# Performance work log

Hardware: AMD Instinct MI355X
Metric: run time of the kernel (lower is better)

## Reference

```python
import jax, jax.numpy as jnp
import numpy as np

NUM_GROUPS = 32
EPS = 1e-6


def group_norm(x, w, b):
    # x: (B, C, L); normalize per group of C//32 channels over (channels-in-group, L)
    B, C, L = x.shape
    xg = x.reshape(B, NUM_GROUPS, C // NUM_GROUPS, L)
    mean = jnp.mean(xg, axis=(2, 3), keepdims=True)
    var = jnp.var(xg, axis=(2, 3), keepdims=True)
    xn = ((xg - mean) * jax.lax.rsqrt(var + EPS)).reshape(B, C, L)
    return xn * w[None, :, None] + b[None, :, None]


def conv1x1(x, w, b):
    # 1x1 Conv1d == channel-mixing linear. x: (B,C,L), w: (O,C), b: (O,)
    return jnp.einsum('oc,bcl->bol', w, x) + b[None, :, None]


def setup_inputs() -> dict:
    key = jax.random.key(0)
    ks = jax.random.split(key, 6)
    B, C, L = 8, 512, 2048
    s = 1.0 / np.sqrt(C)
    return {
        'x': jax.random.normal(ks[0], (B, C, L), dtype=jnp.float32),
        'gn_w': jnp.ones((C,), jnp.float32),
        'gn_b': jnp.zeros((C,), jnp.float32),
        'wq': jax.random.normal(ks[1], (C, C), dtype=jnp.float32) * s,
        'bq': jnp.zeros((C,), jnp.float32),
        'wk': jax.random.normal(ks[2], (C, C), dtype=jnp.float32) * s,
        'bk': jnp.zeros((C,), jnp.float32),
        'wv': jax.random.normal(ks[3], (C, C), dtype=jnp.float32) * s,
        'bv': jnp.zeros((C,), jnp.float32),
        'wo': jax.random.normal(ks[4], (C, C), dtype=jnp.float32) * s,
        'bo': jnp.zeros((C,), jnp.float32),
    }


def reference(x, gn_w, gn_b, wq, bq, wk, bk, wv, bv, wo, bo):
    B, C, L = x.shape
    h = group_norm(x, gn_w, gn_b)
    q = conv1x1(h, wq, bq)  # (B,C,L)
    k = conv1x1(h, wk, bk)
    v = conv1x1(h, wv, bv)
    scale = jnp.asarray(C, x.dtype) ** -0.5
    # scores over length: w[b,i,j] = sum_c q[b,c,i] k[b,c,j]
    w_ = jnp.einsum('bci,bcj->bij', q, k) * scale
    w_ = jax.nn.softmax(w_, axis=-1)
    # h[b,c,i] = sum_j w[b,i,j] v[b,c,j]
    h = jnp.einsum('bij,bcj->bci', w_, v)
    h = conv1x1(h, wo, bo)
    return x + h
```

## Files before the change

### kernel.cpp

```cpp
#include <hip/hip_runtime.h>
#include <math.h>

#define BATCH 8
#define CH 512
#define LEN 2048
#define NG 32
#define CPG 16

typedef unsigned short u16;
typedef __bf16 bf16x8 __attribute__((ext_vector_type(8)));
typedef float f32x16 __attribute__((ext_vector_type(16)));

__device__ __forceinline__ u16 f2bf(float f) {
    union { float f; unsigned u; } c; c.f = f;
    unsigned r = c.u + 0x7fffu + ((c.u >> 16) & 1u);
    return (u16)(r >> 16);
}
__device__ __forceinline__ float bf2f(u16 h) {
    union { unsigned u; float f; } c; c.u = ((unsigned)h) << 16;
    return c.f;
}
__device__ __forceinline__ void gload16(const u16* g, u16* l) {
    __builtin_amdgcn_global_load_lds(
        (const __attribute__((address_space(1))) unsigned int*)g,
        (__attribute__((address_space(3))) unsigned int*)l, 16, 0, 0);
}

__global__ __launch_bounds__(256) void zerof4(float4* __restrict__ p) {
    p[blockIdx.x * 256 + threadIdx.x] = make_float4(0.f, 0.f, 0.f, 0.f);
}

__global__ __launch_bounds__(256) void wconv4(const float* __restrict__ w0, const float* __restrict__ w1,
                                              const float* __restrict__ w2, const float* __restrict__ w3,
                                              u16* __restrict__ o0, u16* __restrict__ o1,
                                              u16* __restrict__ o2, u16* __restrict__ o3) {
    const float* s; u16* d;
    switch (blockIdx.y) {
        case 0: s = w0; d = o0; break;
        case 1: s = w1; d = o1; break;
        case 2: s = w2; d = o2; break;
        default: s = w3; d = o3; break;
    }
    const int i = blockIdx.x * 256 + threadIdx.x;
    float4 f = ((const float4*)s)[i];
    ushort4 o = make_ushort4(f2bf(f.x), f2bf(f.y), f2bf(f.z), f2bf(f.w));
    ((ushort4*)d)[i] = o;
}

__global__ __launch_bounds__(256) void gn_stats(const float* __restrict__ x,
                                                const float* __restrict__ gw,
                                                const float* __restrict__ gb,
                                                float* __restrict__ gnA,
                                                float* __restrict__ gnB) {
    const int b = blockIdx.x >> 5, g = blockIdx.x & 31;
    const float4* xp = (const float4*)(x + ((size_t)b * CH + (size_t)g * CPG) * LEN);
    float s = 0.f, s2 = 0.f;
    for (int i = threadIdx.x; i < (CPG * LEN) / 4; i += 256) {
        float4 v = xp[i];
        s += v.x + v.y + v.z + v.w;
        s2 = fmaf(v.x, v.x, fmaf(v.y, v.y, fmaf(v.z, v.z, fmaf(v.w, v.w, s2))));
    }
    #pragma unroll
    for (int off = 32; off > 0; off >>= 1) {
        s  += __shfl_down(s, off, 64);
        s2 += __shfl_down(s2, off, 64);
    }
    __shared__ float sm[2][4];
    const int lane = threadIdx.x & 63, wv = threadIdx.x >> 6;
    if (lane == 0) { sm[0][wv] = s; sm[1][wv] = s2; }
    __syncthreads();
    if (threadIdx.x < CPG) {
        const float S  = sm[0][0] + sm[0][1] + sm[0][2] + sm[0][3];
        const float S2 = sm[1][0] + sm[1][1] + sm[1][2] + sm[1][3];
        const float mean = S * (1.f / (CPG * LEN));
        const float var  = S2 * (1.f / (CPG * LEN)) - mean * mean;
        const float rstd = rsqrtf(var + 1e-6f);
        const int c = g * CPG + threadIdx.x;
        const float sc = rstd * gw[c];
        gnA[b * CH + c] = sc;
        gnB[b * CH + c] = gb[c] - mean * sc;
    }
}

__global__ __launch_bounds__(256) void gn_apply_t(const float* __restrict__ x,
                                                  const float* __restrict__ gnA,
                                                  const float* __restrict__ gnB,
                                                  u16* __restrict__ Ht) {
    __shared__ float tile[64][65];
    const int b = blockIdx.z, c0 = blockIdx.y * 64, l0 = blockIdx.x * 64;
    const int t = threadIdx.x, tl = t & 63, tr = t >> 6;
    #pragma unroll 4
    for (int i = 0; i < 16; ++i) {
        const int c = tr + i * 4;
        const float a = gnA[b * CH + c0 + c];
        const float sh = gnB[b * CH + c0 + c];
        tile[c][tl] = x[((size_t)b * CH + c0 + c) * LEN + l0 + tl] * a + sh;
    }
    __syncthreads();
    #pragma unroll 4
    for (int i = 0; i < 16; ++i) {
        const int l = tr + i * 4;
        Ht[((size_t)b * LEN + l0 + l) * CH + c0 + tl] = f2bf(tile[tl][l]);
    }
}

#define EPI_QK   0
#define EPI_TBN  1
#define EPI_EXP  2
#define EPI_TNRM 3
#define EPI_FIN  4

template <int MODE>
__global__ __launch_bounds__(256) void gemm_bt(
    const u16* __restrict__ A, int lda, long long sA,
    const u16* __restrict__ B, int ldb, long long sB,
    void* __restrict__ Out, void* __restrict__ Out2,
    int ldo, long long sO,
    const float* __restrict__ bias, const float* __restrict__ bias2,
    const float* __restrict__ res, long long sR,
    float* __restrict__ rsum, long long sRS,
    int K, float alpha) {
    __shared__ u16 As[128 * 64];
    __shared__ u16 Bs[128 * 64];
    const int b = blockIdx.z;
    const int n0 = blockIdx.x * 128, m0 = blockIdx.y * 128;
    A += (size_t)b * sA;
    B += (size_t)b * sB;
    const int t = threadIdx.x;
    const int lane = t & 63, wid = t >> 6;

    const int rowL = t >> 3, kq = (t & 7) ^ (rowL & 7);
    const u16* gA[4];
    const u16* gB[4];
    u16* lA[4];
    u16* lB[4];
    #pragma unroll
    for (int g = 0; g < 4; ++g) {
        gA[g] = A + (size_t)(m0 + rowL + g * 32) * lda + kq * 8;
        gB[g] = B + (size_t)(n0 + rowL + g * 32) * ldb + kq * 8;
        lA[g] = As + t * 8 + g * 2048;
        lB[g] = Bs + t * 8 + g * 2048;
    }

    f32x16 acc[2][2];
    #pragma unroll
    for (int i = 0; i < 2; ++i)
        #pragma unroll
        for (int j = 0; j < 2; ++j)
            acc[i][j] = (f32x16)(0.f);

    const int col = lane & 31, half = lane >> 5;
    const int wm = (wid & 1) * 64, wn = (wid >> 1) * 64;
    const int mf = wm + col, nf = wn + col;
    const int mswz = mf & 7, nswz = nf & 7;

    for (int k0 = 0; k0 < K; k0 += 64) {
        #pragma unroll
        for (int g = 0; g < 4; ++g) {
            gload16(gA[g], lA[g]);
            gload16(gB[g], lB[g]);
            gA[g] += 64; gB[g] += 64;
        }
        __syncthreads();
        #pragma unroll
        for (int ks = 0; ks < 4; ++ks) {
            const int kcA = ((ks * 2 + half) ^ mswz) * 8;
            const int kcB = ((ks * 2 + half) ^ nswz) * 8;
            bf16x8 a0 = *(const bf16x8*)(As + (mf)      * 64 + kcA);
            bf16x8 a1 = *(const bf16x8*)(As + (mf + 32) * 64 + kcA);
            bf16x8 b0 = *(const bf16x8*)(Bs + (nf)      * 64 + kcB);
            bf16x8 b1 = *(const bf16x8*)(Bs + (nf + 32) * 64 + kcB);
            acc[0][0] = __builtin_amdgcn_mfma_f32_32x32x16_bf16(a0, b0, acc[0][0], 0, 0, 0);
            acc[0][1] = __builtin_amdgcn_mfma_f32_32x32x16_bf16(a0, b1, acc[0][1], 0, 0, 0);
            acc[1][0] = __builtin_amdgcn_mfma_f32_32x32x16_bf16(a1, b0, acc[1][0], 0, 0, 0);
            acc[1][1] = __builtin_amdgcn_mfma_f32_32x32x16_bf16(a1, b1, acc[1][1], 0, 0, 0);
        }
        __syncthreads();
    }

    if (MODE == EPI_FIN) {
        float* O = (float*)Out + (size_t)b * sO;
        const float* R = res + (size_t)b * sR;
        #pragma unroll
        for (int im = 0; im < 2; ++im)
            #pragma unroll
            for (int g4 = 0; g4 < 4; ++g4) {
                const int mb = m0 + wm + im * 32 + g4 * 8 + half * 4;
                #pragma unroll
                for (int jn = 0; jn < 2; ++jn) {
                    const int n = n0 + wn + jn * 32 + col;
                    const float bb = bias[n];
                    const size_t base = (size_t)n * ldo + mb;
                    const float4 r4 = *(const float4*)&R[base];
                    float4 o4;
                    o4.x = acc[im][jn][g4 * 4 + 0] + bb + r4.x;
                    o4.y = acc[im][jn][g4 * 4 + 1] + bb + r4.y;
                    o4.z = acc[im][jn][g4 * 4 + 2] + bb + r4.z;
                    o4.w = acc[im][jn][g4 * 4 + 3] + bb + r4.w;
                    *(float4*)&O[base] = o4;
                }
            }
    } else if (MODE == EPI_EXP) {
        u16* O = (u16*)Out + (size_t)b * sO;
        float* RS = rsum + (size_t)b * sRS;
        float psum[2] = {0.f, 0.f};
        #pragma unroll
        for (int im = 0; im < 2; ++im)
            #pragma unroll
            for (int g4 = 0; g4 < 4; ++g4) {
                const int mb = m0 + wm + im * 32 + g4 * 8 + half * 4;
                #pragma unroll
                for (int jn = 0; jn < 2; ++jn) {
                    const int n = n0 + wn + jn * 32 + col;
                    u16 h0 = f2bf(__expf(acc[im][jn][g4 * 4 + 0] * alpha));
                    u16 h1 = f2bf(__expf(acc[im][jn][g4 * 4 + 1] * alpha));
                    u16 h2 = f2bf(__expf(acc[im][jn][g4 * 4 + 2] * alpha));
                    u16 h3 = f2bf(__expf(acc[im][jn][g4 * 4 + 3] * alpha));
                    psum[jn] += bf2f(h0) + bf2f(h1) + bf2f(h2) + bf2f(h3);
                    *(ushort4*)&O[(size_t)n * ldo + mb] = make_ushort4(h0, h1, h2, h3);
                }
            }
        #pragma unroll
        for (int jn = 0; jn < 2; ++jn) psum[jn] += __shfl_xor(psum[jn], 32, 64);
        if (half == 0) {
            #pragma unroll
            for (int jn = 0; jn < 2; ++jn)
                atomicAdd(&RS[n0 + wn + jn * 32 + col], psum[jn]);
        }
    } else {
        u16* O;
        const float* bi = bias;
        const float* RS = (MODE == EPI_TNRM) ? rsum + (size_t)b * sRS : nullptr;
        int mbase = m0 + wm;
        if (MODE == EPI_QK) {
            const bool hi = (m0 & 512) != 0;
            O  = (u16*)(hi ? Out2 : Out) + (size_t)b * sO;
            bi = hi ? bias2 : bias;
            mbase = (m0 & 511) + wm;
        } else {
            O = (u16*)Out + (size_t)b * sO;
        }
        float inv[2];
        if (MODE == EPI_TNRM) {
            inv[0] = 1.f / RS[n0 + wn + col];
            inv[1] = 1.f / RS[n0 + wn + 32 + col];
        }
        #pragma unroll
        for (int im = 0; im < 2; ++im)
            #pragma unroll
            for (int g4 = 0; g4 < 4; ++g4) {
                const int mb = mbase + im * 32 + g4 * 8 + half * 4;
                float4 bm = make_float4(0.f, 0.f, 0.f, 0.f);
                if (MODE == EPI_QK) bm = *(const float4*)&bi[mb];
                #pragma unroll
                for (int jn = 0; jn < 2; ++jn) {
                    const int n = n0 + wn + jn * 32 + col;
                    float v0 = acc[im][jn][g4 * 4 + 0];
                    float v1 = acc[im][jn][g4 * 4 + 1];
                    float v2 = acc[im][jn][g4 * 4 + 2];
                    float v3 = acc[im][jn][g4 * 4 + 3];
                    if (MODE == EPI_QK)  { v0 += bm.x; v1 += bm.y; v2 += bm.z; v3 += bm.w; }
                    if (MODE == EPI_TBN) { const float bb = bi[n]; v0 += bb; v1 += bb; v2 += bb; v3 += bb; }
                    if (MODE == EPI_TNRM) { v0 *= inv[jn]; v1 *= inv[jn]; v2 *= inv[jn]; v3 *= inv[jn]; }
                    ushort4 pk = make_ushort4(f2bf(v0), f2bf(v1), f2bf(v2), f2bf(v3));
                    *(ushort4*)&O[(size_t)n * ldo + mb] = pk;
                }
            }
    }
}

extern "C" void kernel_launch(void* const* d_in, const int* in_sizes, int n_in,
                              void* d_out, int out_size, void* d_ws, size_t ws_size,
                              hipStream_t stream) {
    const float* x    = (const float*)d_in[0];
    const float* gn_w = (const float*)d_in[1];
    const float* gn_b = (const float*)d_in[2];
    const float* wq   = (const float*)d_in[3];
    const float* bq   = (const float*)d_in[4];
    const float* wk   = (const float*)d_in[5];
    const float* bk   = (const float*)d_in[6];
    const float* wv   = (const float*)d_in[7];
    const float* bv   = (const float*)d_in[8];
    const float* wo   = (const float*)d_in[9];
    const float* bo   = (const float*)d_in[10];
    float* out = (float*)d_out;

    char* p = (char*)d_ws;
    const size_t WSZ = (size_t)CH * CH * 2;
    const size_t HSZ = (size_t)BATCH * CH * LEN * 2;
    u16* Wqk = (u16*)p; p += 2 * WSZ;
    u16* Wvb = (u16*)p; p += WSZ;
    u16* Wob = (u16*)p; p += WSZ;
    u16* Ht  = (u16*)p; p += HSZ;
    u16* Qt  = (u16*)p; p += HSZ;
    u16* Kt  = (u16*)p; p += HSZ;
    u16* Vb  = (u16*)p; p += HSZ;
    u16* Sb  = (u16*)p; p += (size_t)BATCH * LEN * LEN * 2;
    float* gnA = (float*)p; p += (size_t)BATCH * CH * 4;
    float* gnB = (float*)p; p += (size_t)BATCH * CH * 4;
    float* rowsum = (float*)p;

    const long long sH = (long long)LEN * CH;
    const long long sV = (long long)CH * LEN;
    const long long sS = (long long)LEN * LEN;
    const float scale = 0.04419417382415922f;

    wconv4<<<dim3(256, 4), 256, 0, stream>>>(wq, wk, wv, wo,
                                             Wqk, Wqk + (size_t)CH * CH, Wvb, Wob);
    gn_stats<<<BATCH * NG, 256, 0, stream>>>(x, gn_w, gn_b, gnA, gnB);
    gn_apply_t<<<dim3(LEN / 64, CH / 64, BATCH), 256, 0, stream>>>(x, gnA, gnB, Ht);
    zerof4<<<BATCH * LEN / 1024, 256, 0, stream>>>((float4*)rowsum);

    gemm_bt<EPI_QK><<<dim3(16, 8, 8), 256, 0, stream>>>(
        Wqk, CH, 0, Ht, CH, sH, Qt, Kt, CH, sH, bq, bk, nullptr, 0, nullptr, 0, CH, 0.f);
    gemm_bt<EPI_TBN><<<dim3(4, 16, 8), 256, 0, stream>>>(
        Ht, CH, sH, Wvb, CH, 0, Vb, nullptr, LEN, sV, bv, nullptr, nullptr, 0, nullptr, 0, CH, 0.f);
    gemm_bt<EPI_EXP><<<dim3(16, 16, 8), 256, 0, stream>>>(
        Kt, CH, sH, Qt, CH, sH, Sb, nullptr, LEN, sS, nullptr, nullptr, nullptr, 0, rowsum, LEN, CH, scale);
    gemm_bt<EPI_TNRM><<<dim3(16, 4, 8), 256, 0, stream>>>(
        Vb, LEN, sV, Sb, LEN, sS, Ht, nullptr, CH, sH, nullptr, nullptr, nullptr, 0, rowsum, LEN, LEN, 0.f);
    gemm_bt<EPI_FIN><<<dim3(4, 16, 8), 256, 0, stream>>>(
        Ht, CH, sH, Wob, CH, 0, out, nullptr, LEN, sV, bo, nullptr, x, sV, nullptr, 0, CH, 0.f);
}
```

Measured before the change: 301.8 us.

## Use 256x128 tile GEMM for QK projection and scores; merge prep kernels

Adds a gemm_big kernel with a 256x128 output tile (4x2 MFMA 32x32 fragments per wave) and uses it for the fused Q/K projection and the exp(QK^T) score GEMM. The larger tile raises arithmetic intensity and halves the block count for those launches. The weight conversion, group-norm statistics and rowsum zeroing are also merged into one prep launch to save launch overhead. The trade-offs are higher register and LDS use per block, which may lower occupancy, and fewer blocks per launch.

```diff
diff --git a/kernel.cpp b/kernel.cpp
--- a/kernel.cpp
+++ b/kernel.cpp
@@ -26,59 +26,57 @@
         (__attribute__((address_space(3))) unsigned int*)l, 16, 0, 0);
 }
 
-__global__ __launch_bounds__(256) void zerof4(float4* __restrict__ p) {
-    p[blockIdx.x * 256 + threadIdx.x] = make_float4(0.f, 0.f, 0.f, 0.f);
-}
-
-__global__ __launch_bounds__(256) void wconv4(const float* __restrict__ w0, const float* __restrict__ w1,
-                                              const float* __restrict__ w2, const float* __restrict__ w3,
-                                              u16* __restrict__ o0, u16* __restrict__ o1,
-                                              u16* __restrict__ o2, u16* __restrict__ o3) {
-    const float* s; u16* d;
-    switch (blockIdx.y) {
-        case 0: s = w0; d = o0; break;
-        case 1: s = w1; d = o1; break;
-        case 2: s = w2; d = o2; break;
-        default: s = w3; d = o3; break;
-    }
-    const int i = blockIdx.x * 256 + threadIdx.x;
-    float4 f = ((const float4*)s)[i];
-    ushort4 o = make_ushort4(f2bf(f.x), f2bf(f.y), f2bf(f.z), f2bf(f.w));
-    ((ushort4*)d)[i] = o;
-}
-
-__global__ __launch_bounds__(256) void gn_stats(const float* __restrict__ x,
-                                                const float* __restrict__ gw,
-                                                const float* __restrict__ gb,
-                                                float* __restrict__ gnA,
-                                                float* __restrict__ gnB) {
-    const int b = blockIdx.x >> 5, g = blockIdx.x & 31;
-    const float4* xp = (const float4*)(x + ((size_t)b * CH + (size_t)g * CPG) * LEN);
-    float s = 0.f, s2 = 0.f;
-    for (int i = threadIdx.x; i < (CPG * LEN) / 4; i += 256) {
-        float4 v = xp[i];
-        s += v.x + v.y + v.z + v.w;
-        s2 = fmaf(v.x, v.x, fmaf(v.y, v.y, fmaf(v.z, v.z, fmaf(v.w, v.w, s2))));
-    }
-    #pragma unroll
-    for (int off = 32; off > 0; off >>= 1) {
-        s  += __shfl_down(s, off, 64);
-        s2 += __shfl_down(s2, off, 64);
-    }
-    __shared__ float sm[2][4];
-    const int lane = threadIdx.x & 63, wv = threadIdx.x >> 6;
-    if (lane == 0) { sm[0][wv] = s; sm[1][wv] = s2; }
-    __syncthreads();
-    if (threadIdx.x < CPG) {
-        const float S  = sm[0][0] + sm[0][1] + sm[0][2] + sm[0][3];
-        const float S2 = sm[1][0] + sm[1][1] + sm[1][2] + sm[1][3];
-        const float mean = S * (1.f / (CPG * LEN));
-        const float var  = S2 * (1.f / (CPG * LEN)) - mean * mean;
-        const float rstd = rsqrtf(var + 1e-6f);
-        const int c = g * CPG + threadIdx.x;
-        const float sc = rstd * gw[c];
-        gnA[b * CH + c] = sc;
-        gnB[b * CH + c] = gb[c] - mean * sc;
+__global__ __launch_bounds__(256) void prep(
+    const float* __restrict__ wq, const float* __restrict__ wk,
+    const float* __restrict__ wv, const float* __restrict__ wo,
+    u16* __restrict__ Wqk, u16* __restrict__ Wvb, u16* __restrict__ Wob,
+    const float* __restrict__ x, const float* __restrict__ gw,
+    const float* __restrict__ gb, float* __restrict__ gnA,
+    float* __restrict__ gnB, float4* __restrict__ rsz) {
+    const int blk = blockIdx.x, t = threadIdx.x;
+    if (blk < 1024) {
+        const float* s; u16* d;
+        switch (blk >> 8) {
+            case 0: s = wq; d = Wqk; break;
+            case 1: s = wk; d = Wqk + (size_t)CH * CH; break;
+            case 2: s = wv; d = Wvb; break;
+            default: s = wo; d = Wob; break;
+        }
+        const int i = (blk & 255) * 256 + t;
+        float4 f = ((const float4*)s)[i];
+        ((ushort4*)d)[i] = make_ushort4(f2bf(f.x), f2bf(f.y), f2bf(f.z), f2bf(f.w));
+    } else if (blk < 1280) {
+        const int bg = blk - 1024;
+        const int b = bg >> 5, g = bg & 31;
+        const float4* xp = (const float4*)(x + ((size_t)b * CH + (size_t)g * CPG) * LEN);
+        float s = 0.f, s2 = 0.f;
+        for (int i = t; i < (CPG * LEN) / 4; i += 256) {
+            float4 v = xp[i];
+            s += v.x + v.y + v.z + v.w;
+            s2 = fmaf(v.x, v.x, fmaf(v.y, v.y, fmaf(v.z, v.z, fmaf(v.w, v.w, s2))));
+        }
+        #pragma unroll
+        for (int off = 32; off > 0; off >>= 1) {
+            s  += __shfl_down(s, off, 64);
+            s2 += __shfl_down(s2, off, 64);
+        }
+        __shared__ float sm[2][4];
+        const int lane = t & 63, wv4 = t >> 6;
+        if (lane == 0) { sm[0][wv4] = s; sm[1][wv4] = s2; }
+        __syncthreads();
+        if (t < CPG) {
+            const float S  = sm[0][0] + sm[0][1] + sm[0][2] + sm[0][3];
+            const float S2 = sm[1][0] + sm[1][1] + sm[1][2] + sm[1][3];
+            const float mean = S * (1.f / (CPG * LEN));
+            const float var  = S2 * (1.f / (CPG * LEN)) - mean * mean;
+            const float rstd = rsqrtf(var + 1e-6f);
+            const int c = g * CPG + t;
+            const float sc = rstd * gw[c];
+            gnA[b * CH + c] = sc;
+            gnB[b * CH + c] = gb[c] - mean * sc;
+        }
+    } else {
+        rsz[(blk - 1280) * 256 + t] = make_float4(0.f, 0.f, 0.f, 0.f);
     }
 }
 
@@ -200,12 +198,116 @@
                     *(float4*)&O[base] = o4;
                 }
             }
-    } else if (MODE == EPI_EXP) {
+    } else {
+        u16* O = (u16*)Out + (size_t)b * sO;
+        const float* bi = bias;
+        const float* RS = (MODE == EPI_TNRM) ? rsum + (size_t)b * sRS : nullptr;
+        float inv[2];
+        if (MODE == EPI_TNRM) {
+            inv[0] = 1.f / RS[n0 + wn + col];
+            inv[1] = 1.f / RS[n0 + wn + 32 + col];
+        }
+        #pragma unroll
+        for (int im = 0; im < 2; ++im)
+            #pragma unroll
+            for (int g4 = 0; g4 < 4; ++g4) {
+                const int mb = m0 + wm + im * 32 + g4 * 8 + half * 4;
+                #pragma unroll
+                for (int jn = 0; jn < 2; ++jn) {
+                    const int n = n0 + wn + jn * 32 + col;
+                    float v0 = acc[im][jn][g4 * 4 + 0];
+                    float v1 = acc[im][jn][g4 * 4 + 1];
+                    float v2 = acc[im][jn][g4 * 4 + 2];
+                    float v3 = acc[im][jn][g4 * 4 + 3];
+                    if (MODE == EPI_TBN) { const float bb = bi[n]; v0 += bb; v1 += bb; v2 += bb; v3 += bb; }
+                    if (MODE == EPI_TNRM) { v0 *= inv[jn]; v1 *= inv[jn]; v2 *= inv[jn]; v3 *= inv[jn]; }
+                    ushort4 pk = make_ushort4(f2bf(v0), f2bf(v1), f2bf(v2), f2bf(v3));
+                    *(ushort4*)&O[(size_t)n * ldo + mb] = pk;
+                }
+            }
+    }
+}
+
+template <int MODE>
+__global__ __launch_bounds__(256) void gemm_big(
+    const u16* __restrict__ A, int lda, long long sA,
+    const u16* __restrict__ B, int ldb, long long sB,
+    void* __restrict__ Out, void* __restrict__ Out2,
+    int ldo, long long sO,
+    const float* __restrict__ bias, const float* __restrict__ bias2,
+    float* __restrict__ rsum, long long sRS,
+    int K, float alpha) {
+    __shared__ u16 As[256 * 64];
+    __shared__ u16 Bs[128 * 64];
+    const int b = blockIdx.z;
+    const int n0 = blockIdx.x * 128, m0 = blockIdx.y * 256;
+    A += (size_t)b * sA;
+    B += (size_t)b * sB;
+    const int t = threadIdx.x;
+    const int lane = t & 63, wid = t >> 6;
+
+    const int rowL = t >> 3, kq = (t & 7) ^ (rowL & 7);
+    const u16* gA[8];
+    const u16* gB[4];
+    u16* lA[8];
+    u16* lB[4];
+    #pragma unroll
+    for (int g = 0; g < 8; ++g) {
+        gA[g] = A + (size_t)(m0 + rowL + g * 32) * lda + kq * 8;
+        lA[g] = As + t * 8 + g * 2048;
+    }
+    #pragma unroll
+    for (int g = 0; g < 4; ++g) {
+        gB[g] = B + (size_t)(n0 + rowL + g * 32) * ldb + kq * 8;
+        lB[g] = Bs + t * 8 + g * 2048;
+    }
+
+    f32x16 acc[4][2];
+    #pragma unroll
+    for (int i = 0; i < 4; ++i)
+        #pragma unroll
+        for (int j = 0; j < 2; ++j)
+            acc[i][j] = (f32x16)(0.f);
+
+    const int col = lane & 31, half = lane >> 5;
+    const int wm = (wid & 1) * 128, wn = (wid >> 1) * 64;
+    const int mf = wm + col, nf = wn + col;
+    const int mswz = mf & 7, nswz = nf & 7;
+
+    for (int k0 = 0; k0 < K; k0 += 64) {
+        #pragma unroll
+        for (int g = 0; g < 8; ++g) { gload16(gA[g], lA[g]); gA[g] += 64; }
+        #pragma unroll
+        for (int g = 0; g < 4; ++g) { gload16(gB[g], lB[g]); gB[g] += 64; }
+        __syncthreads();
+        #pragma unroll
+        for (int ks = 0; ks < 4; ++ks) {
+            const int kcA = ((ks * 2 + half) ^ mswz) * 8;
+            const int kcB = ((ks * 2 + half) ^ nswz) * 8;
+            bf16x8 a0 = *(const bf16x8*)(As + (mf)      * 64 + kcA);
+            bf16x8 a1 = *(const bf16x8*)(As + (mf + 32) * 64 + kcA);
+            bf16x8 a2 = *(const bf16x8*)(As + (mf + 64) * 64 + kcA);
+            bf16x8 a3 = *(const bf16x8*)(As + (mf + 96) * 64 + kcA);
+            bf16x8 b0 = *(const bf16x8*)(Bs + (nf)      * 64 + kcB);
+            bf16x8 b1 = *(const bf16x8*)(Bs + (nf + 32) * 64 + kcB);
+            acc[0][0] = __builtin_amdgcn_mfma_f32_32x32x16_bf16(a0, b0, acc[0][0], 0, 0, 0);
+            acc[0][1] = __builtin_amdgcn_mfma_f32_32x32x16_bf16(a0, b1, acc[0][1], 0, 0, 0);
+            acc[1][0] = __builtin_amdgcn_mfma_f32_32x32x16_bf16(a1, b0, acc[1][0], 0, 0, 0);
+            acc[1][1] = __builtin_amdgcn_mfma_f32_32x32x16_bf16(a1, b1, acc[1][1], 0, 0, 0);
+            acc[2][0] = __builtin_amdgcn_mfma_f32_32x32x16_bf16(a2, b0, acc[2][0], 0, 0, 0);
+            acc[2][1] = __builtin_amdgcn_mfma_f32_32x32x16_bf16(a2, b1, acc[2][1], 0, 0, 0);
+            acc[3][0] = __builtin_amdgcn_mfma_f32_32x32x16_bf16(a3, b0, acc[3][0], 0, 0, 0);
+            acc[3][1] = __builtin_amdgcn_mfma_f32_32x32x16_bf16(a3, b1, acc[3][1], 0, 0, 0);
+        }
+        __syncthreads();
+    }
+
+    if (MODE == EPI_EXP) {
         u16* O = (u16*)Out + (size_t)b * sO;
         float* RS = rsum + (size_t)b * sRS;
         float psum[2] = {0.f, 0.f};
         #pragma unroll
-        for (int im = 0; im < 2; ++im)
+        for (int im = 0; im < 4; ++im)
             #pragma unroll
             for (int g4 = 0; g4 < 4; ++g4) {
                 const int mb = m0 + wm + im * 32 + g4 * 8 + half * 4;
@@ -228,41 +330,23 @@
                 atomicAdd(&RS[n0 + wn + jn * 32 + col], psum[jn]);
         }
     } else {
-        u16* O;
-        const float* bi = bias;
-        const float* RS = (MODE == EPI_TNRM) ? rsum + (size_t)b * sRS : nullptr;
-        int mbase = m0 + wm;
-        if (MODE == EPI_QK) {
-            const bool hi = (m0 & 512) != 0;
-            O  = (u16*)(hi ? Out2 : Out) + (size_t)b * sO;
-            bi = hi ? bias2 : bias;
-            mbase = (m0 & 511) + wm;
-        } else {
-            O = (u16*)Out + (size_t)b * sO;
-        }
-        float inv[2];
-        if (MODE == EPI_TNRM) {
-            inv[0] = 1.f / RS[n0 + wn + col];
-            inv[1] = 1.f / RS[n0 + wn + 32 + col];
-        }
-        #pragma unroll
-        for (int im = 0; im < 2; ++im)
+        const bool hi = (m0 & 512) != 0;
+        u16* O = (u16*)(hi ? Out2 : Out) + (size_t)b * sO;
+        const float* bi = hi ? bias2 : bias;
+        const int mbase = (m0 & 511) + wm;
+        #pragma unroll
+        for (int im = 0; im < 4; ++im)
             #pragma unroll
             for (int g4 = 0; g4 < 4; ++g4) {
                 const int mb = mbase + im * 32 + g4 * 8 + half * 4;
-                float4 bm = make_float4(0.f, 0.f, 0.f, 0.f);
-                if (MODE == EPI_QK) bm = *(const float4*)&bi[mb];
+                const float4 bm = *(const float4*)&bi[mb];
                 #pragma unroll
                 for (int jn = 0; jn < 2; ++jn) {
                     const int n = n0 + wn + jn * 32 + col;
-                    float v0 = acc[im][jn][g4 * 4 + 0];
-                    float v1 = acc[im][jn][g4 * 4 + 1];
-                    float v2 = acc[im][jn][g4 * 4 + 2];
-                    float v3 = acc[im][jn][g4 * 4 + 3];
-                    if (MODE == EPI_QK)  { v0 += bm.x; v1 += bm.y; v2 += bm.z; v3 += bm.w; }
-                    if (MODE == EPI_TBN) { const float bb = bi[n]; v0 += bb; v1 += bb; v2 += bb; v3 += bb; }
-                    if (MODE == EPI_TNRM) { v0 *= inv[jn]; v1 *= inv[jn]; v2 *= inv[jn]; v3 *= inv[jn]; }
-                    ushort4 pk = make_ushort4(f2bf(v0), f2bf(v1), f2bf(v2), f2bf(v3));
+                    ushort4 pk = make_ushort4(f2bf(acc[im][jn][g4 * 4 + 0] + bm.x),
+                                              f2bf(acc[im][jn][g4 * 4 + 1] + bm.y),
+                                              f2bf(acc[im][jn][g4 * 4 + 2] + bm.z),
+                                              f2bf(acc[im][jn][g4 * 4 + 3] + bm.w));
                     *(ushort4*)&O[(size_t)n * ldo + mb] = pk;
                 }
             }
@@ -305,18 +389,16 @@
     const long long sS = (long long)LEN * LEN;
     const float scale = 0.04419417382415922f;
 
-    wconv4<<<dim3(256, 4), 256, 0, stream>>>(wq, wk, wv, wo,
-                                             Wqk, Wqk + (size_t)CH * CH, Wvb, Wob);
-    gn_stats<<<BATCH * NG, 256, 0, stream>>>(x, gn_w, gn_b, gnA, gnB);
+    prep<<<1296, 256, 0, stream>>>(wq, wk, wv, wo, Wqk, Wvb, Wob,
+                                   x, gn_w, gn_b, gnA, gnB, (float4*)rowsum);
     gn_apply_t<<<dim3(LEN / 64, CH / 64, BATCH), 256, 0, stream>>>(x, gnA, gnB, Ht);
-    zerof4<<<BATCH * LEN / 1024, 256, 0, stream>>>((float4*)rowsum);
-
-    gemm_bt<EPI_QK><<<dim3(16, 8, 8), 256, 0, stream>>>(
-        Wqk, CH, 0, Ht, CH, sH, Qt, Kt, CH, sH, bq, bk, nullptr, 0, nullptr, 0, CH, 0.f);
+
+    gemm_big<EPI_QK><<<dim3(16, 4, 8), 256, 0, stream>>>(
+        Wqk, CH, 0, Ht, CH, sH, Qt, Kt, CH, sH, bq, bk, nullptr, 0, CH, 0.f);
     gemm_bt<EPI_TBN><<<dim3(4, 16, 8), 256, 0, stream>>>(
         Ht, CH, sH, Wvb, CH, 0, Vb, nullptr, LEN, sV, bv, nullptr, nullptr, 0, nullptr, 0, CH, 0.f);
-    gemm_bt<EPI_EXP><<<dim3(16, 16, 8), 256, 0, stream>>>(
-        Kt, CH, sH, Qt, CH, sH, Sb, nullptr, LEN, sS, nullptr, nullptr, nullptr, 0, rowsum, LEN, CH, scale);
+    gemm_big<EPI_EXP><<<dim3(16, 8, 8), 256, 0, stream>>>(
+        Kt, CH, sH, Qt, CH, sH, Sb, nullptr, LEN, sS, nullptr, nullptr, rowsum, LEN, CH, scale);
     gemm_bt<EPI_TNRM><<<dim3(16, 4, 8), 256, 0, stream>>>(
         Vb, LEN, sV, Sb, LEN, sS, Ht, nullptr, CH, sH, nullptr, nullptr, nullptr, 0, rowsum, LEN, LEN, 0.f);
     gemm_bt<EPI_FIN><<<dim3(4, 16, 8), 256, 0, stream>>>(
```

Result: slower. 327.4 us (+8.5%).
